# Optimization experiments

Hardware: AMD Instinct MI355X
Metric: run time of the kernel (lower is better)

Reference implementation:

```python
import jax, jax.numpy as jnp
import numpy as np

B, IN, OUT = 8192, 4096, 4096
EPS = 1e-4


def setup_inputs() -> dict:
    key = jax.random.key(0)
    k1, k2 = jax.random.split(key)
    x = jax.random.normal(k1, (B, IN), dtype=jnp.float32)
    gamma = jnp.ones((IN,), dtype=jnp.float32)
    beta = jnp.zeros((IN,), dtype=jnp.float32)
    weight = jax.random.normal(k2, (OUT, IN), dtype=jnp.float32) * 0.02
    bias = jnp.zeros((OUT,), dtype=jnp.float32)
    return {"x": x, "gamma": gamma, "beta": beta, "weight": weight, "bias": bias}


def bin_weight(w):
    # center per output row, clamp, L1-scale, sign (2D branch of BinWeightFn)
    wc = jnp.clip(w - jnp.mean(w, axis=1, keepdims=True), -1.0, 1.0)
    n = w.shape[1]
    scale = jnp.sum(jnp.abs(wc), axis=1, keepdims=True) / n  # [out, 1]
    return jnp.sign(wc), scale


def reference(x, gamma, beta, weight, bias):
    # BatchNorm1d in training mode: batch statistics (biased variance)
    mu = jnp.mean(x, axis=0)
    var = jnp.var(x, axis=0)
    xn = (x - mu) / jnp.sqrt(var + EPS) * gamma + beta
    # binarize activations and weights
    x_bin = jnp.sign(xn)
    w_bin, scale = bin_weight(weight)
    # binary GEMM + bias, then per-output-channel L1 scale, then ReLU
    y = x_bin @ w_bin.T + bias          # [B, OUT]
    y = y * scale.reshape(1, -1)
    return jax.nn.relu(y)
```

## Files before the change

### kernel.cpp

```cpp
#include <hip/hip_runtime.h>
#include <stdint.h>

#define BATCH 8192
#define IN 4096
#define OUT 4096
#define EPS 1e-4f
#define RCHUNK 128
#define NCHUNKS (BATCH / RCHUNK)

typedef int v4i __attribute__((ext_vector_type(4)));
typedef unsigned char u8;

#define AS1(p) ((const __attribute__((address_space(1))) void*)(p))
#define AS3(p) ((__attribute__((address_space(3))) void*)(p))

__global__ __launch_bounds__(256) void colstat_partial(
    const float* __restrict__ x, float* __restrict__ P1, float* __restrict__ P2) {
    int c4 = blockIdx.x * 256 + threadIdx.x;
    int r0 = blockIdx.y * RCHUNK;
    float4 s1 = {0.f, 0.f, 0.f, 0.f}, s2 = {0.f, 0.f, 0.f, 0.f};
    const float4* p = (const float4*)x + (size_t)r0 * (IN / 4) + c4;
#pragma unroll 8
    for (int r = 0; r < RCHUNK; ++r) {
        float4 v = p[(size_t)r * (IN / 4)];
        s1.x += v.x; s1.y += v.y; s1.z += v.z; s1.w += v.w;
        s2.x += v.x * v.x; s2.y += v.y * v.y; s2.z += v.z * v.z; s2.w += v.w * v.w;
    }
    ((float4*)P1)[blockIdx.y * (IN / 4) + c4] = s1;
    ((float4*)P2)[blockIdx.y * (IN / 4) + c4] = s2;
}

__global__ __launch_bounds__(256) void colstat_final(
    const float* __restrict__ P1, const float* __restrict__ P2,
    const float* __restrict__ gamma, float* __restrict__ mu, float* __restrict__ aArr) {
    int col = blockIdx.x * 256 + threadIdx.x;
    double s1 = 0.0, s2 = 0.0;
#pragma unroll 4
    for (int c = 0; c < NCHUNKS; ++c) {
        s1 += (double)P1[c * IN + col];
        s2 += (double)P2[c * IN + col];
    }
    double m = s1 / (double)BATCH;
    double var = s2 / (double)BATCH - m * m;
    float rstd = (float)(1.0 / sqrt(var + (double)EPS));
    mu[col] = (float)m;
    aArr[col] = rstd * gamma[col];
}

__global__ __launch_bounds__(256) void binxw(
    const float* __restrict__ x, const float* __restrict__ mu,
    const float* __restrict__ aArr, const float* __restrict__ beta,
    const float* __restrict__ w,
    u8* __restrict__ x01, int* __restrict__ px,
    u8* __restrict__ w01, float* __restrict__ scale, int* __restrict__ pw) {
    __shared__ double redd[4];
    __shared__ int redi[4];
    __shared__ double bcast;
    int tid = threadIdx.x;
    int lane = tid & 63;
    int wv = tid >> 6;

    if (blockIdx.x < OUT) {
        int o = blockIdx.x;
        const float4* row = (const float4*)(w + (size_t)o * IN);
        uchar4* o4 = (uchar4*)(w01 + (size_t)o * IN);

        float4 vs[4];
        float part = 0.f;
#pragma unroll
        for (int it = 0; it < 4; ++it) {
            vs[it] = row[it * 256 + tid];
            part += vs[it].x + vs[it].y + vs[it].z + vs[it].w;
        }
        double d = (double)part;
        for (int off = 32; off > 0; off >>= 1) d += __shfl_down(d, off, 64);
        if (lane == 0) redd[wv] = d;
        __syncthreads();
        if (tid == 0) bcast = (redd[0] + redd[1] + redd[2] + redd[3]) / (double)IN;
        __syncthreads();
        float mean = (float)bcast;

        float absacc = 0.f;
        int cnt = 0;
#pragma unroll
        for (int it = 0; it < 4; ++it) {
            float4 v = vs[it];
            float wcx = v.x - mean, wcy = v.y - mean, wcz = v.z - mean, wcw = v.w - mean;
            uchar4 ob;
            ob.x = (u8)(wcx > 0.f);
            ob.y = (u8)(wcy > 0.f);
            ob.z = (u8)(wcz > 0.f);
            ob.w = (u8)(wcw > 0.f);
            cnt += (int)ob.x + (int)ob.y + (int)ob.z + (int)ob.w;
            absacc += fminf(fabsf(wcx), 1.0f) + fminf(fabsf(wcy), 1.0f) +
                      fminf(fabsf(wcz), 1.0f) + fminf(fabsf(wcw), 1.0f);
            o4[it * 256 + tid] = ob;
        }
        double da = (double)absacc;
        for (int off = 32; off > 0; off >>= 1) da += __shfl_down(da, off, 64);
        for (int off = 32; off > 0; off >>= 1) cnt += __shfl_down(cnt, off, 64);
        if (lane == 0) { redd[wv] = da; redi[wv] = cnt; }
        __syncthreads();
        if (tid == 0) {
            scale[o] = (float)((redd[0] + redd[1] + redd[2] + redd[3]) / (double)IN);
            pw[o] = redi[0] + redi[1] + redi[2] + redi[3];
        }
    } else {
        int r = blockIdx.x - OUT;
        const float4* row = (const float4*)(x + (size_t)r * IN);
        const float4* m4 = (const float4*)mu;
        const float4* a4 = (const float4*)aArr;
        const float4* b4 = (const float4*)beta;
        uchar4* o4 = (uchar4*)(x01 + (size_t)r * IN);
        int cnt = 0;
#pragma unroll
        for (int it = 0; it < IN / 1024; ++it) {
            int q = it * 256 + tid;
            float4 v = row[q];
            float4 m = m4[q];
            float4 a = a4[q];
            float4 b = b4[q];
            uchar4 ob;
            ob.x = (u8)((v.x - m.x) * a.x + b.x > 0.f);
            ob.y = (u8)((v.y - m.y) * a.y + b.y > 0.f);
            ob.z = (u8)((v.z - m.z) * a.z + b.z > 0.f);
            ob.w = (u8)((v.w - m.w) * a.w + b.w > 0.f);
            cnt += (int)ob.x + (int)ob.y + (int)ob.z + (int)ob.w;
            o4[q] = ob;
        }
        for (int off = 32; off > 0; off >>= 1) cnt += __shfl_down(cnt, off, 64);
        if (lane == 0) redi[wv] = cnt;
        __syncthreads();
        if (tid == 0) px[r] = redi[0] + redi[1] + redi[2] + redi[3];
    }
}

#define BKB 128
#define NKT (IN / BKB)
#define NIT (NKT / 2)

#define STG_A(t, q, p) __builtin_amdgcn_global_load_lds( \
    AS1(ag + (size_t)((q)*64 + slr) * IN + (t)*BKB + sswz), \
    AS3(lds + (p)*65536 + (q)*8192 + sdst), 16, 0, 0)
#define STG_B(t, q, p) __builtin_amdgcn_global_load_lds( \
    AS1(bg + (size_t)((q)*64 + slr) * IN + (t)*BKB + sswz), \
    AS3(lds + (p)*65536 + 32768 + (q)*8192 + sdst), 16, 0, 0)

#define LOADA(p, rh) do { \
    _Pragma("unroll") for (int i_ = 0; i_ < 4; ++i_) \
    _Pragma("unroll") for (int k_ = 0; k_ < 2; ++k_) \
        af[i_][k_] = *(const v4i*)(lds + (p)*65536 + aBase + (rh)*8192 + i_*2048 + swk[k_]); \
} while (0)
#define LOADB(p, ch, arr) do { \
    _Pragma("unroll") for (int j_ = 0; j_ < 2; ++j_) \
    _Pragma("unroll") for (int k_ = 0; k_ < 2; ++k_) \
        arr[j_][k_] = *(const v4i*)(lds + (p)*65536 + bBase + (ch)*4096 + j_*2048 + swk[k_]); \
} while (0)
#define MMA(rh, ch, arr) do { \
    __builtin_amdgcn_s_setprio(1); \
    _Pragma("unroll") for (int i_ = 0; i_ < 4; ++i_) \
    _Pragma("unroll") for (int j_ = 0; j_ < 2; ++j_) \
    _Pragma("unroll") for (int k_ = 0; k_ < 2; ++k_) \
        acc[(rh)*4 + i_][(ch)*2 + j_] = __builtin_amdgcn_mfma_i32_16x16x64_i8( \
            af[i_][k_], arr[j_][k_], acc[(rh)*4 + i_][(ch)*2 + j_], 0, 0, 0); \
    __builtin_amdgcn_s_setprio(0); \
} while (0)
#define BAR() asm volatile("s_barrier" ::: "memory")
#define VM(n) asm volatile("s_waitcnt vmcnt(" #n ")" ::: "memory")

__global__ __launch_bounds__(512, 2) void bgemm_i8(
    const u8* __restrict__ x01, const u8* __restrict__ w01,
    const int* __restrict__ px, const int* __restrict__ pw,
    const float* __restrict__ scale, const float* __restrict__ bias,
    float* __restrict__ out) {
    __shared__ u8 lds[131072];

    int tid = threadIdx.x;
    int lane = tid & 63;
    int wave = tid >> 6;
    int wm = wave >> 2;
    int wn = wave & 3;

    int lin = blockIdx.y * (OUT / 256) + blockIdx.x;
    int swz = (lin & 7) * 64 + (lin >> 3);
    int colBlk = (swz & 15) * 256;
    int rowBlk = (swz >> 4) * 256;

    const u8* ag = x01 + (size_t)rowBlk * IN;
    const u8* bg = w01 + (size_t)colBlk * IN;

    int slr = tid >> 3;
    int ss = tid & 7;
    int sswz = (ss ^ (slr & 7)) * 16;
    int sdst = slr * 128 + ss * 16;

    int lrow = lane & 15;
    int lhi = lane >> 4;
    int llo = lane & 7;
    int swk[2] = { ((lhi) ^ llo) * 16, ((4 + lhi) ^ llo) * 16 };
    int aBase = (wm * 128 + lrow) * 128;
    int bBase = 32768 + (wn * 64 + lrow) * 128;

    v4i acc[8][4];
#pragma unroll
    for (int i = 0; i < 8; ++i)
#pragma unroll
        for (int j = 0; j < 4; ++j) acc[i][j] = (v4i){0, 0, 0, 0};
    v4i af[4][2], bf0[2][2], bf1[2][2];

    STG_A(0, 0, 0); STG_A(0, 2, 0);
    STG_B(0, 0, 0); STG_B(0, 1, 0); STG_B(0, 2, 0); STG_B(0, 3, 0);
    STG_A(0, 1, 0); STG_A(0, 3, 0);
    STG_A(1, 0, 1); STG_A(1, 2, 1);
    STG_B(1, 0, 1); STG_B(1, 1, 1); STG_B(1, 2, 1); STG_B(1, 3, 1);
    STG_A(1, 1, 1); STG_A(1, 3, 1);
    VM(10);
    BAR();

    for (int j = 0; j < NIT - 1; ++j) {
        int E2 = 2 * j + 2, O2 = 2 * j + 3;
        LOADA(0, 0); LOADB(0, 0, bf0);
        BAR(); MMA(0, 0, bf0); BAR();
        LOADB(0, 1, bf1);
        STG_A(E2, 0, 0); STG_A(E2, 2, 0);
        BAR(); MMA(0, 1, bf1); VM(8); BAR();
        LOADA(0, 1);
        STG_B(E2, 0, 0); STG_B(E2, 1, 0); STG_B(E2, 2, 0); STG_B(E2, 3, 0);
        BAR(); MMA(1, 0, bf0); BAR();
        STG_A(E2, 1, 0); STG_A(E2, 3, 0);
        BAR(); MMA(1, 1, bf1); VM(10); BAR();
        LOADA(1, 0); LOADB(1, 0, bf0);
        BAR(); MMA(0, 0, bf0); BAR();
        LOADB(1, 1, bf1);
        STG_A(O2, 0, 1); STG_A(O2, 2, 1);
        BAR(); MMA(0, 1, bf1); VM(8); BAR();
        LOADA(1, 1);
        STG_B(O2, 0, 1); STG_B(O2, 1, 1); STG_B(O2, 2, 1); STG_B(O2, 3, 1);
        BAR(); MMA(1, 0, bf0); BAR();
        STG_A(O2, 1, 1); STG_A(O2, 3, 1);
        BAR(); MMA(1, 1, bf1); VM(10); BAR();
    }

    {
        LOADA(0, 0); LOADB(0, 0, bf0);
        BAR(); MMA(0, 0, bf0); BAR();
        LOADB(0, 1, bf1);
        BAR(); MMA(0, 1, bf1); VM(8); BAR();
        LOADA(0, 1);
        BAR(); MMA(1, 0, bf0); BAR();
        BAR(); MMA(1, 1, bf1); VM(2); BAR();
        LOADA(1, 0); LOADB(1, 0, bf0);
        BAR(); MMA(0, 0, bf0); BAR();
        LOADB(1, 1, bf1);
        BAR(); MMA(0, 1, bf1); VM(0); BAR();
        LOADA(1, 1);
        BAR(); MMA(1, 0, bf0); BAR();
        BAR(); MMA(1, 1, bf1); BAR();
    }

    int crow0 = lhi * 4;
    int ccol = lrow;
#pragma unroll
    for (int i = 0; i < 8; ++i) {
        int rbase = rowBlk + wm * 128 + i * 16 + crow0;
        int pxr[4];
#pragma unroll
        for (int rg = 0; rg < 4; ++rg) pxr[rg] = px[rbase + rg];
#pragma unroll
        for (int j = 0; j < 4; ++j) {
            int cb = colBlk + wn * 64 + j * 16 + ccol;
            float sc = scale[cb];
            float bs = bias[cb];
            int pwc = pw[cb];
#pragma unroll
            for (int rg = 0; rg < 4; ++rg) {
                int dot = 4 * acc[i][j][rg] - 2 * pxr[rg] - 2 * pwc + IN;
                float y = ((float)dot + bs) * sc;
                out[(size_t)(rbase + rg) * OUT + cb] = y > 0.f ? y : 0.f;
            }
        }
    }
}

extern "C" void kernel_launch(void* const* d_in, const int* in_sizes, int n_in,
                              void* d_out, int out_size, void* d_ws, size_t ws_size,
                              hipStream_t stream) {
    const float* x = (const float*)d_in[0];
    const float* gamma = (const float*)d_in[1];
    const float* beta = (const float*)d_in[2];
    const float* weight = (const float*)d_in[3];
    const float* bias = (const float*)d_in[4];
    float* out = (float*)d_out;

    char* w = (char*)d_ws;
    float* mu = (float*)(w);
    float* aArr = (float*)(w + 16384);
    float* scale = (float*)(w + 32768);
    int* px = (int*)(w + 49152);
    int* pw = (int*)(w + 81920);
    float* P1 = (float*)(w + (1 << 20));
    float* P2 = (float*)(w + (2 << 20));
    u8* x01 = (u8*)(w + (4 << 20));
    u8* w01 = (u8*)(w + (36 << 20));

    colstat_partial<<<dim3(IN / 1024, NCHUNKS), 256, 0, stream>>>(x, P1, P2);
    colstat_final<<<dim3(IN / 256), 256, 0, stream>>>(P1, P2, gamma, mu, aArr);
    binxw<<<dim3(OUT + BATCH), 256, 0, stream>>>(x, mu, aArr, beta, weight,
                                                 x01, px, w01, scale, pw);
    bgemm_i8<<<dim3(OUT / 256, BATCH / 256), 512, 0, stream>>>(x01, w01, px, pw, scale, bias, out);
}
```

Baseline: 400.7 us.

## Replace double-buffered K=128 GEMM loop with 4-stage K=64 LDS ring

Restructures the int8 MFMA main loop. The old schedule staged 128-wide K tiles into two LDS buffers with interleaved half-tile loads and many barriers. The new one stages 64-wide K tiles into a four-slot ring, prefetching three tiles ahead, with one barrier and one vmcnt wait per step. It also changes the LDS XOR swizzle to suit 64-byte rows. The aim is to cut barrier overhead and deepen load latency hiding, at the cost of more loop steps and a new swizzle whose bank-conflict behaviour is untested.

```diff
diff --git a/kernel.cpp b/kernel.cpp
--- a/kernel.cpp
+++ b/kernel.cpp
@@ -135,36 +135,34 @@
     }
 }
 
-#define BKB 128
-#define NKT (IN / BKB)
-#define NIT (NKT / 2)
-
-#define STG_A(t, q, p) __builtin_amdgcn_global_load_lds( \
-    AS1(ag + (size_t)((q)*64 + slr) * IN + (t)*BKB + sswz), \
-    AS3(lds + (p)*65536 + (q)*8192 + sdst), 16, 0, 0)
-#define STG_B(t, q, p) __builtin_amdgcn_global_load_lds( \
-    AS1(bg + (size_t)((q)*64 + slr) * IN + (t)*BKB + sswz), \
-    AS3(lds + (p)*65536 + 32768 + (q)*8192 + sdst), 16, 0, 0)
-
-#define LOADA(p, rh) do { \
-    _Pragma("unroll") for (int i_ = 0; i_ < 4; ++i_) \
-    _Pragma("unroll") for (int k_ = 0; k_ < 2; ++k_) \
-        af[i_][k_] = *(const v4i*)(lds + (p)*65536 + aBase + (rh)*8192 + i_*2048 + swk[k_]); \
+#define BK2 64
+#define NT2 (IN / BK2)
+
+#define STG2_A(t, q) __builtin_amdgcn_global_load_lds( \
+    AS1(ag + (size_t)((q)*128 + slr2) * IN + (t)*BK2 + sswz2), \
+    AS3(lds + ((t)&3)*32768 + (q)*8192 + sdst2), 16, 0, 0)
+#define STG2_B(t, q) __builtin_amdgcn_global_load_lds( \
+    AS1(bg + (size_t)((q)*128 + slr2) * IN + (t)*BK2 + sswz2), \
+    AS3(lds + ((t)&3)*32768 + 16384 + (q)*8192 + sdst2), 16, 0, 0)
+#define STG2(t) do { STG2_A(t,0); STG2_A(t,1); STG2_B(t,0); STG2_B(t,1); } while (0)
+
+#define RD(t) do { \
+    const u8* bp_ = lds + ((t)&3)*32768; \
+    _Pragma("unroll") for (int j_ = 0; j_ < 4; ++j_) \
+        bf[j_] = *(const v4i*)(bp_ + bB + j_*1024); \
+    _Pragma("unroll") for (int i_ = 0; i_ < 8; ++i_) \
+        af[i_] = *(const v4i*)(bp_ + aB + i_*1024); \
 } while (0)
-#define LOADB(p, ch, arr) do { \
-    _Pragma("unroll") for (int j_ = 0; j_ < 2; ++j_) \
-    _Pragma("unroll") for (int k_ = 0; k_ < 2; ++k_) \
-        arr[j_][k_] = *(const v4i*)(lds + (p)*65536 + bBase + (ch)*4096 + j_*2048 + swk[k_]); \
-} while (0)
-#define MMA(rh, ch, arr) do { \
+
+#define MMA2() do { \
     __builtin_amdgcn_s_setprio(1); \
-    _Pragma("unroll") for (int i_ = 0; i_ < 4; ++i_) \
-    _Pragma("unroll") for (int j_ = 0; j_ < 2; ++j_) \
-    _Pragma("unroll") for (int k_ = 0; k_ < 2; ++k_) \
-        acc[(rh)*4 + i_][(ch)*2 + j_] = __builtin_amdgcn_mfma_i32_16x16x64_i8( \
-            af[i_][k_], arr[j_][k_], acc[(rh)*4 + i_][(ch)*2 + j_], 0, 0, 0); \
+    _Pragma("unroll") for (int i_ = 0; i_ < 8; ++i_) \
+    _Pragma("unroll") for (int j_ = 0; j_ < 4; ++j_) \
+        acc[i_][j_] = __builtin_amdgcn_mfma_i32_16x16x64_i8( \
+            af[i_], bf[j_], acc[i_][j_], 0, 0, 0); \
     __builtin_amdgcn_s_setprio(0); \
 } while (0)
+
 #define BAR() asm volatile("s_barrier" ::: "memory")
 #define VM(n) asm volatile("s_waitcnt vmcnt(" #n ")" ::: "memory")
 
@@ -189,74 +187,46 @@
     const u8* ag = x01 + (size_t)rowBlk * IN;
     const u8* bg = w01 + (size_t)colBlk * IN;
 
-    int slr = tid >> 3;
-    int ss = tid & 7;
-    int sswz = (ss ^ (slr & 7)) * 16;
-    int sdst = slr * 128 + ss * 16;
+    int slr2 = tid >> 2;
+    int ss2 = tid & 3;
+    int sxor = (slr2 & 3) ^ ((slr2 >> 2) & 3);
+    int sswz2 = (ss2 ^ sxor) * 16;
+    int sdst2 = slr2 * 64 + ss2 * 16;
 
     int lrow = lane & 15;
     int lhi = lane >> 4;
-    int llo = lane & 7;
-    int swk[2] = { ((lhi) ^ llo) * 16, ((4 + lhi) ^ llo) * 16 };
-    int aBase = (wm * 128 + lrow) * 128;
-    int bBase = 32768 + (wn * 64 + lrow) * 128;
+    int rxor = (lrow & 3) ^ ((lrow >> 2) & 3);
+    int swk2 = (lhi ^ rxor) * 16;
+    int aB = (wm * 128 + lrow) * 64 + swk2;
+    int bB = 16384 + (wn * 64 + lrow) * 64 + swk2;
 
     v4i acc[8][4];
 #pragma unroll
     for (int i = 0; i < 8; ++i)
 #pragma unroll
         for (int j = 0; j < 4; ++j) acc[i][j] = (v4i){0, 0, 0, 0};
-    v4i af[4][2], bf0[2][2], bf1[2][2];
-
-    STG_A(0, 0, 0); STG_A(0, 2, 0);
-    STG_B(0, 0, 0); STG_B(0, 1, 0); STG_B(0, 2, 0); STG_B(0, 3, 0);
-    STG_A(0, 1, 0); STG_A(0, 3, 0);
-    STG_A(1, 0, 1); STG_A(1, 2, 1);
-    STG_B(1, 0, 1); STG_B(1, 1, 1); STG_B(1, 2, 1); STG_B(1, 3, 1);
-    STG_A(1, 1, 1); STG_A(1, 3, 1);
-    VM(10);
+    v4i af[8], bf[4];
+
+    STG2(0); STG2(1); STG2(2);
+    VM(8);
     BAR();
 
-    for (int j = 0; j < NIT - 1; ++j) {
-        int E2 = 2 * j + 2, O2 = 2 * j + 3;
-        LOADA(0, 0); LOADB(0, 0, bf0);
-        BAR(); MMA(0, 0, bf0); BAR();
-        LOADB(0, 1, bf1);
-        STG_A(E2, 0, 0); STG_A(E2, 2, 0);
-        BAR(); MMA(0, 1, bf1); VM(8); BAR();
-        LOADA(0, 1);
-        STG_B(E2, 0, 0); STG_B(E2, 1, 0); STG_B(E2, 2, 0); STG_B(E2, 3, 0);
-        BAR(); MMA(1, 0, bf0); BAR();
-        STG_A(E2, 1, 0); STG_A(E2, 3, 0);
-        BAR(); MMA(1, 1, bf1); VM(10); BAR();
-        LOADA(1, 0); LOADB(1, 0, bf0);
-        BAR(); MMA(0, 0, bf0); BAR();
-        LOADB(1, 1, bf1);
-        STG_A(O2, 0, 1); STG_A(O2, 2, 1);
-        BAR(); MMA(0, 1, bf1); VM(8); BAR();
-        LOADA(1, 1);
-        STG_B(O2, 0, 1); STG_B(O2, 1, 1); STG_B(O2, 2, 1); STG_B(O2, 3, 1);
-        BAR(); MMA(1, 0, bf0); BAR();
-        STG_A(O2, 1, 1); STG_A(O2, 3, 1);
-        BAR(); MMA(1, 1, bf1); VM(10); BAR();
-    }
-
-    {
-        LOADA(0, 0); LOADB(0, 0, bf0);
-        BAR(); MMA(0, 0, bf0); BAR();
-        LOADB(0, 1, bf1);
-        BAR(); MMA(0, 1, bf1); VM(8); BAR();
-        LOADA(0, 1);
-        BAR(); MMA(1, 0, bf0); BAR();
-        BAR(); MMA(1, 1, bf1); VM(2); BAR();
-        LOADA(1, 0); LOADB(1, 0, bf0);
-        BAR(); MMA(0, 0, bf0); BAR();
-        LOADB(1, 1, bf1);
-        BAR(); MMA(0, 1, bf1); VM(0); BAR();
-        LOADA(1, 1);
-        BAR(); MMA(1, 0, bf0); BAR();
-        BAR(); MMA(1, 1, bf1); BAR();
-    }
+    for (int tt = 0; tt < 15; ++tt) {
+        int t0 = tt * 4;
+#pragma unroll
+        for (int u = 0; u < 4; ++u) {
+            int t = t0 + u;
+            RD(t);
+            STG2(t + 3);
+            MMA2();
+            VM(8);
+            BAR();
+        }
+    }
+    RD(60); STG2(63); MMA2(); VM(8); BAR();
+    RD(61); MMA2(); VM(4); BAR();
+    RD(62); MMA2(); VM(0); BAR();
+    RD(63); MMA2();
 
     int crow0 = lhi * 4;
     int ccol = lrow;
```

Measured after the change: 409.4 us. 1.02x slower.
